# Kernel tuning notes

Hardware: AMD Instinct MI355X
Metric: run time of the kernel (lower is better)

## Reference

```python
import jax, jax.numpy as jnp
import numpy as np

MARGIN = 0.2

def _pdist(a, b):
    # euclidean distance matrix, matches pdist_torch (clamp at 1e-12 then sqrt)
    d2 = (a * a).sum(1)[:, None] + (b * b).sum(1)[None, :] - 2.0 * (a @ b.T)
    return jnp.sqrt(jnp.clip(d2, 1e-12))

def setup_inputs() -> dict:
    key = jax.random.key(0)
    P, K, D = 128, 16, 4096  # identities, samples-per-identity, feature dim
    inputs = jax.random.normal(key, (4 * P * K, D), dtype=jnp.float32)
    # labels laid out [modality, identity, sample] so torch.chunk grouping is valid
    targets = jnp.tile(jnp.repeat(jnp.arange(P, dtype=jnp.int64), K), 4)
    return {"inputs": inputs, "targets": targets, "num_classes": P}

def reference(inputs, targets, num_classes):
    P = int(num_classes)
    total, D = inputs.shape
    K = total // (4 * P)
    # per-modality, per-identity centers: [4, P, D]
    c = inputs.reshape(4, P, K, D).mean(axis=2)
    c1, c2, c3, c4 = c[0], c[1], c[2], c[3]

    eye = jnp.eye(P, dtype=bool)
    offdiag_min = lambda d: jnp.min(jnp.where(eye, jnp.inf, d), axis=1)
    # unique labels => mask is identity => masked max/min over mask[i] is the diagonal
    ap123 = jnp.diagonal(_pdist(c2, c3))
    an123 = jax.lax.stop_gradient(jnp.diagonal(_pdist(c1, c3)))  # .detach()
    an33 = offdiag_min(_pdist(c3, c3))
    an11 = offdiag_min(_pdist(c1, c1))
    ap124 = jnp.diagonal(_pdist(c1, c4))
    an124 = jax.lax.stop_gradient(jnp.diagonal(_pdist(c2, c4)))  # .detach()
    an44 = offdiag_min(_pdist(c4, c4))
    an22 = offdiag_min(_pdist(c2, c2))

    # MarginRankingLoss(margin)(x1=an, x2=ap, y=1) = mean(relu(ap - an + margin))
    mrl = lambda an, ap: jnp.mean(jnp.maximum(ap - an + MARGIN, 0.0))
    loss_123 = mrl(an123, ap123) + 0.5 * (mrl(an33, ap123) + mrl(an11, ap123))
    loss_124 = mrl(an124, ap124) + 0.5 * (mrl(an44, ap124) + mrl(an22, ap124))
    return (loss_123 + loss_124) / 2
```

## Files before the change

kernel.cpp:

```cpp
#include <hip/hip_runtime.h>
#include <math.h>

#define P_IDS 128
#define D_DIM 4096
#define K_SMP 16
#define MARGIN_F 0.2f
#define NCHUNK 32
#define NSLAB 16

__global__ __launch_bounds__(256, 4) void k_centers(const float* __restrict__ in,
                                                    float* __restrict__ c,
                                                    float* __restrict__ dpart,
                                                    int* __restrict__ cnt) {
    __shared__ float Lc[4 * 256];
    __shared__ float wred[4][4];
    const int tid = threadIdx.x;
    const int p  = blockIdx.x;
    const int ds = blockIdx.y;
    if (p == 0 && ds == 0 && tid == 0) *cnt = 0;
    const int m = tid >> 6, lane = tid & 63;
    const size_t colbase = (size_t)ds * 256 + lane * 4;

    const float* src = in + (size_t)(m * P_IDS + p) * K_SMP * D_DIM + colbase;
    float4 acc = make_float4(0.f, 0.f, 0.f, 0.f);
    #pragma unroll 4
    for (int k = 0; k < K_SMP; ++k) {
        float4 v = *reinterpret_cast<const float4*>(src + (size_t)k * D_DIM);
        acc.x += v.x; acc.y += v.y; acc.z += v.z; acc.w += v.w;
    }
    const float inv = 1.0f / (float)K_SMP;
    acc.x *= inv; acc.y *= inv; acc.z *= inv; acc.w *= inv;
    *reinterpret_cast<float4*>(c + (size_t)(m * P_IDS + p) * D_DIM + colbase) = acc;
    *reinterpret_cast<float4*>(&Lc[m * 256 + lane * 4]) = acc;
    __syncthreads();

    float v0 = Lc[0 * 256 + tid], v1 = Lc[1 * 256 + tid];
    float v2 = Lc[2 * 256 + tid], v3 = Lc[3 * 256 + tid];
    float d0 = (v1 - v2) * (v1 - v2);
    float d1 = (v0 - v2) * (v0 - v2);
    float d2 = (v0 - v3) * (v0 - v3);
    float d3 = (v1 - v3) * (v1 - v3);
    #pragma unroll
    for (int off = 32; off > 0; off >>= 1) {
        d0 += __shfl_down(d0, off, 64);
        d1 += __shfl_down(d1, off, 64);
        d2 += __shfl_down(d2, off, 64);
        d3 += __shfl_down(d3, off, 64);
    }
    if (lane == 0) { wred[m][0] = d0; wred[m][1] = d1; wred[m][2] = d2; wred[m][3] = d3; }
    __syncthreads();
    if (tid < 4) {
        float s = wred[0][tid] + wred[1][tid] + wred[2][tid] + wred[3][tid];
        dpart[((size_t)ds * 4 + tid) * P_IDS + p] = s;
    }
}

__global__ __launch_bounds__(256) void k_pair(const float* __restrict__ c,
                                              float* __restrict__ part) {
    __shared__ float As[64][68];
    __shared__ float Bs[64][68];
    const int tid = threadIdx.x;
    const int tx = tid & 15, ty = tid >> 4;
    const int bx = blockIdx.x;
    const int m = bx >> 2, it = (bx >> 1) & 1, jt = bx & 1;
    const int dc = blockIdx.y;
    const float* cm = c + (size_t)m * P_IDS * D_DIM;
    const float* gA = cm + (size_t)(it * 64) * D_DIM;
    const float* gB = cm + (size_t)(jt * 64) * D_DIM;

    float acc[4][4];
    #pragma unroll
    for (int r = 0; r < 4; ++r)
        #pragma unroll
        for (int s = 0; s < 4; ++s) acc[r][s] = 0.f;

    for (int ch = 0; ch < 2; ++ch) {
        const int dbase = dc * 128 + ch * 64;
        __syncthreads();
        #pragma unroll
        for (int idx = 0; idx < 4; ++idx) {
            int li = idx * 256 + tid;
            int row = li >> 4, c4 = li & 15;
            *reinterpret_cast<float4*>(&As[row][c4 * 4]) =
                *reinterpret_cast<const float4*>(gA + (size_t)row * D_DIM + dbase + c4 * 4);
            *reinterpret_cast<float4*>(&Bs[row][c4 * 4]) =
                *reinterpret_cast<const float4*>(gB + (size_t)row * D_DIM + dbase + c4 * 4);
        }
        __syncthreads();
        #pragma unroll
        for (int d4 = 0; d4 < 16; ++d4) {
            float4 a[4], b[4];
            #pragma unroll
            for (int r = 0; r < 4; ++r)
                a[r] = *reinterpret_cast<const float4*>(&As[ty * 4 + r][d4 * 4]);
            #pragma unroll
            for (int s = 0; s < 4; ++s)
                b[s] = *reinterpret_cast<const float4*>(&Bs[s * 16 + tx][d4 * 4]);
            #pragma unroll
            for (int r = 0; r < 4; ++r)
                #pragma unroll
                for (int s = 0; s < 4; ++s) {
                    float dx = a[r].x - b[s].x, dy = a[r].y - b[s].y;
                    float dz = a[r].z - b[s].z, dw = a[r].w - b[s].w;
                    acc[r][s] = fmaf(dx, dx, acc[r][s]);
                    acc[r][s] = fmaf(dy, dy, acc[r][s]);
                    acc[r][s] = fmaf(dz, dz, acc[r][s]);
                    acc[r][s] = fmaf(dw, dw, acc[r][s]);
                }
        }
    }
    float* pbase = part + ((size_t)dc * 4 + m) * (P_IDS * P_IDS);
    #pragma unroll
    for (int r = 0; r < 4; ++r) {
        int i = it * 64 + ty * 4 + r;
        #pragma unroll
        for (int s = 0; s < 4; ++s) {
            int j = jt * 64 + s * 16 + tx;
            pbase[i * P_IDS + j] = acc[r][s];
        }
    }
}

__global__ __launch_bounds__(256) void k_tail(const float* __restrict__ part,
                                              const float* __restrict__ dpart,
                                              float* __restrict__ anmin,
                                              int* __restrict__ cnt,
                                              float* __restrict__ out) {
    __shared__ float wmin[4];
    __shared__ float diagf[4 * P_IDS];
    __shared__ float red[4];
    __shared__ int lastflag;
    const int tid = threadIdx.x;
    const int blk = blockIdx.x;

    const int rowid = blk * 2 + (tid >> 7);
    const int j = tid & 127;
    const size_t base = (size_t)rowid * P_IDS + j;
    float sum = 0.f;
    #pragma unroll 4
    for (int dc = 0; dc < NCHUNK; ++dc)
        sum += part[(size_t)dc * 4 * P_IDS * P_IDS + base];
    float d2 = fmaxf(sum, 1e-12f);
    if (j == (rowid & (P_IDS - 1))) d2 = INFINITY;
    #pragma unroll
    for (int off = 32; off > 0; off >>= 1) d2 = fminf(d2, __shfl_down(d2, off, 64));
    if ((tid & 63) == 0) wmin[tid >> 6] = d2;
    __syncthreads();
    if (tid == 0) {
        anmin[blk * 2]     = sqrtf(fminf(wmin[0], wmin[1]));
        anmin[blk * 2 + 1] = sqrtf(fminf(wmin[2], wmin[3]));
        __threadfence();
        lastflag = (atomicAdd(cnt, 1) == 255);
    }
    __syncthreads();

    if (lastflag) {
        __threadfence();
        #pragma unroll
        for (int e = tid; e < 4 * P_IDS; e += 256) {
            float s = 0.f;
            #pragma unroll
            for (int ds = 0; ds < NSLAB; ++ds)
                s += dpart[(size_t)ds * 4 * P_IDS + e];
            diagf[e] = sqrtf(fmaxf(s, 1e-12f));
        }
        __syncthreads();
        float s = 0.f;
        if (tid < 128) {
            const int i = tid;
            float ap123 = diagf[0 * P_IDS + i], an123 = diagf[1 * P_IDS + i];
            float ap124 = diagf[2 * P_IDS + i], an124 = diagf[3 * P_IDS + i];
            float an11 = anmin[0 * P_IDS + i], an22 = anmin[1 * P_IDS + i];
            float an33 = anmin[2 * P_IDS + i], an44 = anmin[3 * P_IDS + i];
            s = fmaxf(ap123 - an123 + MARGIN_F, 0.f)
              + 0.5f * (fmaxf(ap123 - an33 + MARGIN_F, 0.f) +
                        fmaxf(ap123 - an11 + MARGIN_F, 0.f))
              + fmaxf(ap124 - an124 + MARGIN_F, 0.f)
              + 0.5f * (fmaxf(ap124 - an44 + MARGIN_F, 0.f) +
                        fmaxf(ap124 - an22 + MARGIN_F, 0.f));
        }
        #pragma unroll
        for (int off = 32; off > 0; off >>= 1) s += __shfl_down(s, off, 64);
        if ((tid & 63) == 0) red[tid >> 6] = s;
        __syncthreads();
        if (tid == 0)
            out[0] = (red[0] + red[1] + red[2] + red[3]) / (2.0f * (float)P_IDS);
    }
}

extern "C" void kernel_launch(void* const* d_in, const int* in_sizes, int n_in,
                              void* d_out, int out_size, void* d_ws, size_t ws_size,
                              hipStream_t stream) {
    const float* in = (const float*)d_in[0];

    float* c     = (float*)d_ws;
    float* part  = c + (size_t)4 * P_IDS * D_DIM;
    float* dpart = part + (size_t)NCHUNK * 4 * P_IDS * P_IDS;
    float* anmin = dpart + (size_t)NSLAB * 4 * P_IDS;
    int*   cnt   = (int*)(anmin + 4 * P_IDS);
    float* outp  = (float*)d_out;

    hipLaunchKernelGGL(k_centers, dim3(P_IDS, NSLAB), dim3(256), 0, stream,
                       in, c, dpart, cnt);
    hipLaunchKernelGGL(k_pair, dim3(16, NCHUNK), dim3(256), 0, stream, c, part);
    hipLaunchKernelGGL(k_tail, dim3(256), dim3(256), 0, stream,
                       part, dpart, anmin, cnt, outp);
}
```

Baseline: 60.65 us.

## Move cross-modality diagonal distances from centers kernel into tail kernel

The centers kernel becomes a plain mean reduction, with each block covering one (modality, identity) row and 1024 columns, using two independent accumulators. It no longer computes the per-slab diagonal partial distances or needs LDS and barriers for them. The tail kernel gains 128 extra blocks that compute the four cross-modality diagonal distances directly from the centers and write final sqrt values, and the last-block reduction now counts 384 blocks. The aim is a leaner, more bandwidth-friendly centers pass; in exchange the tail re-reads the centers (about 8 MB) and has more blocks to finish.

```diff
diff --git a/kernel.cpp b/kernel.cpp
--- a/kernel.cpp
+++ b/kernel.cpp
@@ -6,53 +6,30 @@
 #define K_SMP 16
 #define MARGIN_F 0.2f
 #define NCHUNK 32
-#define NSLAB 16
 
-__global__ __launch_bounds__(256, 4) void k_centers(const float* __restrict__ in,
-                                                    float* __restrict__ c,
-                                                    float* __restrict__ dpart,
-                                                    int* __restrict__ cnt) {
-    __shared__ float Lc[4 * 256];
-    __shared__ float wred[4][4];
-    const int tid = threadIdx.x;
-    const int p  = blockIdx.x;
+__global__ __launch_bounds__(256) void k_centers(const float* __restrict__ in,
+                                                 float* __restrict__ c,
+                                                 int* __restrict__ cnt) {
+    const int b  = blockIdx.x;
     const int ds = blockIdx.y;
-    if (p == 0 && ds == 0 && tid == 0) *cnt = 0;
-    const int m = tid >> 6, lane = tid & 63;
-    const size_t colbase = (size_t)ds * 256 + lane * 4;
-
-    const float* src = in + (size_t)(m * P_IDS + p) * K_SMP * D_DIM + colbase;
-    float4 acc = make_float4(0.f, 0.f, 0.f, 0.f);
-    #pragma unroll 4
-    for (int k = 0; k < K_SMP; ++k) {
-        float4 v = *reinterpret_cast<const float4*>(src + (size_t)k * D_DIM);
-        acc.x += v.x; acc.y += v.y; acc.z += v.z; acc.w += v.w;
+    const int t  = threadIdx.x;
+    if (b == 0 && ds == 0 && t == 0) *cnt = 0;
+    const float* src = in + (size_t)b * K_SMP * D_DIM + ds * 1024;
+    float* dst = c + (size_t)b * D_DIM + ds * 1024;
+    float4 a0 = make_float4(0.f, 0.f, 0.f, 0.f);
+    float4 a1 = make_float4(0.f, 0.f, 0.f, 0.f);
+    #pragma unroll
+    for (int k = 0; k < K_SMP; k += 2) {
+        float4 v0 = reinterpret_cast<const float4*>(src + (size_t)k * D_DIM)[t];
+        float4 v1 = reinterpret_cast<const float4*>(src + (size_t)(k + 1) * D_DIM)[t];
+        a0.x += v0.x; a0.y += v0.y; a0.z += v0.z; a0.w += v0.w;
+        a1.x += v1.x; a1.y += v1.y; a1.z += v1.z; a1.w += v1.w;
     }
     const float inv = 1.0f / (float)K_SMP;
-    acc.x *= inv; acc.y *= inv; acc.z *= inv; acc.w *= inv;
-    *reinterpret_cast<float4*>(c + (size_t)(m * P_IDS + p) * D_DIM + colbase) = acc;
-    *reinterpret_cast<float4*>(&Lc[m * 256 + lane * 4]) = acc;
-    __syncthreads();
-
-    float v0 = Lc[0 * 256 + tid], v1 = Lc[1 * 256 + tid];
-    float v2 = Lc[2 * 256 + tid], v3 = Lc[3 * 256 + tid];
-    float d0 = (v1 - v2) * (v1 - v2);
-    float d1 = (v0 - v2) * (v0 - v2);
-    float d2 = (v0 - v3) * (v0 - v3);
-    float d3 = (v1 - v3) * (v1 - v3);
-    #pragma unroll
-    for (int off = 32; off > 0; off >>= 1) {
-        d0 += __shfl_down(d0, off, 64);
-        d1 += __shfl_down(d1, off, 64);
-        d2 += __shfl_down(d2, off, 64);
-        d3 += __shfl_down(d3, off, 64);
-    }
-    if (lane == 0) { wred[m][0] = d0; wred[m][1] = d1; wred[m][2] = d2; wred[m][3] = d3; }
-    __syncthreads();
-    if (tid < 4) {
-        float s = wred[0][tid] + wred[1][tid] + wred[2][tid] + wred[3][tid];
-        dpart[((size_t)ds * 4 + tid) * P_IDS + p] = s;
-    }
+    float4 r;
+    r.x = (a0.x + a1.x) * inv; r.y = (a0.y + a1.y) * inv;
+    r.z = (a0.z + a1.z) * inv; r.w = (a0.w + a1.w) * inv;
+    reinterpret_cast<float4*>(dst)[t] = r;
 }
 
 __global__ __launch_bounds__(256) void k_pair(const float* __restrict__ c,
@@ -122,54 +99,68 @@
 }
 
 __global__ __launch_bounds__(256) void k_tail(const float* __restrict__ part,
-                                              const float* __restrict__ dpart,
+                                              const float* __restrict__ c,
                                               float* __restrict__ anmin,
+                                              float* __restrict__ diag,
                                               int* __restrict__ cnt,
                                               float* __restrict__ out) {
-    __shared__ float wmin[4];
-    __shared__ float diagf[4 * P_IDS];
     __shared__ float red[4];
     __shared__ int lastflag;
     const int tid = threadIdx.x;
     const int blk = blockIdx.x;
 
-    const int rowid = blk * 2 + (tid >> 7);
-    const int j = tid & 127;
-    const size_t base = (size_t)rowid * P_IDS + j;
-    float sum = 0.f;
-    #pragma unroll 4
-    for (int dc = 0; dc < NCHUNK; ++dc)
-        sum += part[(size_t)dc * 4 * P_IDS * P_IDS + base];
-    float d2 = fmaxf(sum, 1e-12f);
-    if (j == (rowid & (P_IDS - 1))) d2 = INFINITY;
-    #pragma unroll
-    for (int off = 32; off > 0; off >>= 1) d2 = fminf(d2, __shfl_down(d2, off, 64));
-    if ((tid & 63) == 0) wmin[tid >> 6] = d2;
+    if (blk < 256) {
+        const int rowid = blk * 2 + (tid >> 7);
+        const int j = tid & 127;
+        const size_t base = (size_t)rowid * P_IDS + j;
+        float sum = 0.f;
+        #pragma unroll 4
+        for (int dc = 0; dc < NCHUNK; ++dc)
+            sum += part[(size_t)dc * 4 * P_IDS * P_IDS + base];
+        float d2 = fmaxf(sum, 1e-12f);
+        if (j == (rowid & (P_IDS - 1))) d2 = INFINITY;
+        #pragma unroll
+        for (int off = 32; off > 0; off >>= 1) d2 = fminf(d2, __shfl_down(d2, off, 64));
+        if ((tid & 63) == 0) red[tid >> 6] = d2;
+        __syncthreads();
+        if (tid == 0) {
+            anmin[blk * 2]     = sqrtf(fminf(red[0], red[1]));
+            anmin[blk * 2 + 1] = sqrtf(fminf(red[2], red[3]));
+        }
+    } else {
+        const int i = blk - 256;
+        const int wave = tid >> 6, lane = tid & 63;
+        const int am = (wave == 0 || wave == 3) ? 1 : 0;
+        const int bm = (wave <= 1) ? 2 : 3;
+        const size_t PD = (size_t)P_IDS * D_DIM;
+        const float4* ra = reinterpret_cast<const float4*>(c + am * PD + (size_t)i * D_DIM);
+        const float4* rb = reinterpret_cast<const float4*>(c + bm * PD + (size_t)i * D_DIM);
+        float acc = 0.f;
+        #pragma unroll
+        for (int t = 0; t < 16; ++t) {
+            float4 va = ra[t * 64 + lane];
+            float4 vb = rb[t * 64 + lane];
+            float dx = va.x - vb.x, dy = va.y - vb.y;
+            float dz = va.z - vb.z, dw = va.w - vb.w;
+            acc = fmaf(dx, dx, acc); acc = fmaf(dy, dy, acc);
+            acc = fmaf(dz, dz, acc); acc = fmaf(dw, dw, acc);
+        }
+        #pragma unroll
+        for (int off = 32; off > 0; off >>= 1) acc += __shfl_down(acc, off, 64);
+        if (lane == 0) diag[wave * P_IDS + i] = sqrtf(fmaxf(acc, 1e-12f));
+        __syncthreads();
+    }
+
+    __threadfence();
+    if (tid == 0) lastflag = (atomicAdd(cnt, 1) == 383);
     __syncthreads();
-    if (tid == 0) {
-        anmin[blk * 2]     = sqrtf(fminf(wmin[0], wmin[1]));
-        anmin[blk * 2 + 1] = sqrtf(fminf(wmin[2], wmin[3]));
-        __threadfence();
-        lastflag = (atomicAdd(cnt, 1) == 255);
-    }
-    __syncthreads();
-
     if (lastflag) {
         __threadfence();
-        #pragma unroll
-        for (int e = tid; e < 4 * P_IDS; e += 256) {
-            float s = 0.f;
-            #pragma unroll
-            for (int ds = 0; ds < NSLAB; ++ds)
-                s += dpart[(size_t)ds * 4 * P_IDS + e];
-            diagf[e] = sqrtf(fmaxf(s, 1e-12f));
-        }
-        __syncthreads();
         float s = 0.f;
         if (tid < 128) {
             const int i = tid;
-            float ap123 = diagf[0 * P_IDS + i], an123 = diagf[1 * P_IDS + i];
-            float ap124 = diagf[2 * P_IDS + i], an124 = diagf[3 * P_IDS + i];
+            float ap123 = diag[0 * P_IDS + i], an123 = diag[1 * P_IDS + i];
+            float ap124 = diag[2 * P_IDS + i], an124 = diag[3 * P_IDS + i];
             float an11 = anmin[0 * P_IDS + i], an22 = anmin[1 * P_IDS + i];
             float an33 = anmin[2 * P_IDS + i], an44 = anmin[3 * P_IDS + i];
             s = fmaxf(ap123 - an123 + MARGIN_F, 0.f)
@@ -195,14 +186,14 @@
 
     float* c     = (float*)d_ws;
     float* part  = c + (size_t)4 * P_IDS * D_DIM;
-    float* dpart = part + (size_t)NCHUNK * 4 * P_IDS * P_IDS;
-    float* anmin = dpart + (size_t)NSLAB * 4 * P_IDS;
-    int*   cnt   = (int*)(anmin + 4 * P_IDS);
+    float* anmin = part + (size_t)NCHUNK * 4 * P_IDS * P_IDS;
+    float* diag  = anmin + 4 * P_IDS;
+    int*   cnt   = (int*)(diag + 4 * P_IDS);
     float* outp  = (float*)d_out;
 
-    hipLaunchKernelGGL(k_centers, dim3(P_IDS, NSLAB), dim3(256), 0, stream,
-                       in, c, dpart, cnt);
+    hipLaunchKernelGGL(k_centers, dim3(4 * P_IDS, 4), dim3(256), 0, stream,
+                       in, c, cnt);
     hipLaunchKernelGGL(k_pair, dim3(16, NCHUNK), dim3(256), 0, stream, c, part);
-    hipLaunchKernelGGL(k_tail, dim3(256), dim3(256), 0, stream,
-                       part, dpart, anmin, cnt, outp);
+    hipLaunchKernelGGL(k_tail, dim3(384), dim3(256), 0, stream,
+                       part, c, anmin, diag, cnt, outp);
 }
```

Result: slower. 83.53 us (+37.7%).
